# Performance work log

Measured on AMD Instinct MI355X. Metric: run time of the kernel, lower is better.

Reference implementation:

```python
import jax, jax.numpy as jnp
import numpy as np

H = W = 112  # densepose head output grid
D = 16       # CSE embedding dim


def setup_inputs() -> dict:
    key = jax.random.key(0)
    k1, k2 = jax.random.split(key)
    feats = jax.random.normal(k1, (4, D, H, W), dtype=jnp.float32)
    vertex_embeddings = jax.random.normal(k2, (27554, D), dtype=jnp.float32)
    return {"feats": feats, "vertex_embeddings": vertex_embeddings}


def reference(feats, vertex_embeddings):
    # feats: [bs, 16, 112, 112]; vertex_embeddings: [V, 16]
    c2 = jnp.sum(vertex_embeddings * vertex_embeddings, axis=1)  # [V]

    def per_image(f):
        x = f.reshape(D, -1).T                      # [P, 16], P = 112*112
        x2 = jnp.sum(x * x, axis=1, keepdims=True)  # [P, 1]
        # squared euclidean distance matrix [P, V] (materialized, as in original)
        dist = x2 - 2.0 * (x @ vertex_embeddings.T) + c2[None, :]
        return jnp.argmin(dist, axis=1).reshape(H, W)

    # process images one at a time (matches original per-image loop, bounds peak memory)
    dps = jax.lax.map(per_image, feats)  # [bs, 112, 112] int
    return feats, dps
```

## Files before the change

kernel.cpp:

```cpp
#include <hip/hip_runtime.h>
#include <stdint.h>


#define DIMS   16
#define HW     12544
#define P_TOT  50176
#define V_TOT  27554
#define FEAT_N 802816

#define CV     512
#define NCH    54
#define VPAD   (NCH*CV)
#define PIXW   128
#define TPW    8
#define B2BX   32
#define CNTSTRIDE 32

#define NV     64
#define VC     431
#define PPT    4

typedef __attribute__((ext_vector_type(8))) short bf16x8;
typedef __attribute__((ext_vector_type(4))) float f32x4;

#define OFF_KEYS  0ul
#define OFF_N2MAX 401408ul
#define OFF_C2    401664ul
#define OFF_XN    512000ul
#define OFF_X2T   712704ul
#define OFF_XB    3923968ul
#define OFF_CNT   3923968ul
#define OFF_WB    7135232ul
#define OFF_CM    8904704ul
#define OFF_BKT   19742976ul
#define WS_BIG    30580992ul
#define MOFF_KEYS  0ul
#define MOFF_N2MAX 401408ul
#define MOFF_C2    405504ul
#define MOFF_XN    516096ul
#define MOFF_XB    716800ul
#define MOFF_WB    3928064ul
#define MOFF_CM    5697536ul
#define WS_MID     16535552ul

__device__ __forceinline__ unsigned short rne_bf16(float f) {
    unsigned u = __float_as_uint(f);
    return (unsigned short)((u + 0x7FFFu + ((u >> 16) & 1u)) >> 16);
}
__device__ __forceinline__ float bf2f(unsigned short h) {
    return __uint_as_float(((unsigned)h) << 16);
}
__device__ __forceinline__ unsigned sortable(float s) {
    unsigned u = __float_as_uint(s);
    return (u & 0x80000000u) ? ~u : (u | 0x80000000u);
}

__global__ void prep_v(const float* __restrict__ ve, short* __restrict__ wb,
                       float* __restrict__ c2buf, unsigned* __restrict__ n2max)
{
    int v = blockIdx.x * 256 + threadIdx.x;
    if (v >= VPAD) return;
    int c = v / CV, vl = v % CV;
    bf16x8 r0, r1, r2, r3;
#pragma unroll
    for (int k = 0; k < 8; ++k) { r2[k] = 0; r3[k] = 0; }
    if (v < V_TOT) {
        const float4* w4 = (const float4*)(ve + (size_t)v * DIMS);
        float w[16];
        *(float4*)&w[0] = w4[0]; *(float4*)&w[4]  = w4[1];
        *(float4*)&w[8] = w4[2]; *(float4*)&w[12] = w4[3];
        float c2 = 0.f;
#pragma unroll
        for (int k = 0; k < 16; ++k) c2 = fmaf(w[k], w[k], c2);
        c2buf[v] = c2;
        float n2 = 0.f;
#pragma unroll
        for (int k = 0; k < 16; ++k) {
            unsigned short h = rne_bf16(-2.f * w[k]);
            if (k < 8) r0[k] = (short)h; else r1[k - 8] = (short)h;
            float f = bf2f(h);
            n2 = fmaf(f, f, n2);
        }
        atomicMax(n2max, __float_as_uint(n2));
        unsigned short hi = rne_bf16(c2);
        unsigned short lo = rne_bf16(c2 - bf2f(hi));
        r2[0] = (short)hi; r2[1] = (short)lo;
    } else {
#pragma unroll
        for (int k = 0; k < 8; ++k) { r0[k] = 0; r1[k] = 0; }
        r2[0] = (short)rne_bf16(30000.f);
    }
    *(bf16x8*)(wb + (((size_t)c * 4 + 0) * CV + vl) * 8) = r0;
    *(bf16x8*)(wb + (((size_t)c * 4 + 1) * CV + vl) * 8) = r1;
    *(bf16x8*)(wb + (((size_t)c * 4 + 2) * CV + vl) * 8) = r2;
    *(bf16x8*)(wb + (((size_t)c * 4 + 3) * CV + vl) * 8) = r3;
}

__global__ void prep_x(const float* __restrict__ feats, short* __restrict__ xb,
                       float* __restrict__ xn, float* __restrict__ x2T)
{
    int p = blockIdx.x * 256 + threadIdx.x;
    int b = p / HW, hw = p - b * HW;
    const float* f = feats + (size_t)b * DIMS * HW + hw;
    bf16x8 r0, r1, r2, r3;
#pragma unroll
    for (int k = 0; k < 8; ++k) { r2[k] = 0; r3[k] = 0; }
    float n2 = 0.f;
    float xv[16];
#pragma unroll
    for (int k = 0; k < 16; ++k) {
        float fv = f[k * HW];
        xv[k] = -2.f * fv;
        unsigned short h = rne_bf16(fv);
        if (k < 8) r0[k] = (short)h; else r1[k - 8] = (short)h;
        float x = bf2f(h);
        n2 = fmaf(x, x, n2);
    }
    r2[0] = (short)0x3F80; r2[1] = (short)0x3F80;
    xn[p] = sqrtf(n2);
    if (x2T) {
        float4* o = (float4*)(x2T + (size_t)p * 16);
        o[0] = *(float4*)&xv[0];  o[1] = *(float4*)&xv[4];
        o[2] = *(float4*)&xv[8];  o[3] = *(float4*)&xv[12];
    }
    *(bf16x8*)(xb + ((size_t)0 * P_TOT + p) * 8) = r0;
    *(bf16x8*)(xb + ((size_t)1 * P_TOT + p) * 8) = r1;
    *(bf16x8*)(xb + ((size_t)2 * P_TOT + p) * 8) = r2;
    *(bf16x8*)(xb + ((size_t)3 * P_TOT + p) * 8) = r3;
}

__global__ __launch_bounds__(256)
void pass_a(const short* __restrict__ xb, const short* __restrict__ wb,
            float* __restrict__ chunkmin)
{
    __shared__ int4 wlds[4 * CV];
    const int c = blockIdx.y;
    const int4* wsrc = (const int4*)(wb + (size_t)c * 4 * CV * 8);
    for (int r = threadIdx.x; r < 4 * CV; r += 256) wlds[r] = wsrc[r];

    const int wid = threadIdx.x >> 6, lane = threadIdx.x & 63;
    const int q = lane >> 4, l15 = lane & 15;
    const int p0 = (blockIdx.x * 4 + wid) * PIXW;

    bf16x8 bfrag[TPW];
#pragma unroll
    for (int t = 0; t < TPW; ++t)
        bfrag[t] = *(const bf16x8*)(xb + ((size_t)q * P_TOT + p0 + t * 16 + l15) * 8);

    __syncthreads();

    f32x4 z = {0.f, 0.f, 0.f, 0.f};
    float run[TPW];
#pragma unroll
    for (int t = 0; t < TPW; ++t) run[t] = 3.0e38f;

    const short* wl = (const short*)wlds + (size_t)q * CV * 8;
#pragma unroll 2
    for (int s = 0; s < CV / 16; ++s) {
        bf16x8 a = *(const bf16x8*)(wl + (s * 16 + l15) * 8);
        f32x4 acc[TPW];
#pragma unroll
        for (int t = 0; t < TPW; ++t)
            acc[t] = __builtin_amdgcn_mfma_f32_16x16x32_bf16(a, bfrag[t], z, 0, 0, 0);
#pragma unroll
        for (int t = 0; t < TPW; ++t) {
            float m = fminf(fminf(acc[t][0], acc[t][1]), acc[t][2]);
            run[t] = fminf(fminf(run[t], acc[t][3]), m);
        }
    }
#pragma unroll
    for (int t = 0; t < TPW; ++t) {
        float v = run[t];
        v = fminf(v, __shfl_xor(v, 16, 64));
        v = fminf(v, __shfl_xor(v, 32, 64));
        if (lane < 16)
            chunkmin[(size_t)c * P_TOT + p0 + t * 16 + lane] = v;
    }
}

__global__ __launch_bounds__(256)
void pass_b1(const float* __restrict__ chunkmin, const float* __restrict__ xn,
             const unsigned* __restrict__ n2max,
             unsigned* __restrict__ cnt, unsigned* __restrict__ buckets)
{
    __shared__ unsigned hist[NCH];
    __shared__ unsigned basech[NCH];
    __shared__ unsigned offch[NCH];

    const int tid  = threadIdx.x;
    const int p    = blockIdx.x * 256 + tid;
    const int lane = tid & 63;

    for (int i = tid; i < NCH; i += 256) { hist[i] = 0; offch[i] = 0; }
    __syncthreads();

    float cm[NCH];
    float gm = 3.0e38f;
#pragma unroll
    for (int c = 0; c < NCH; ++c) {
        cm[c] = chunkmin[(size_t)c * P_TOT + p];
        gm = fminf(gm, cm[c]);
    }
    float Wm = sqrtf(__uint_as_float(*n2max));
    float T = gm + 2.f * (0.004f * xn[p] * Wm + 1e-3f);

#pragma unroll
    for (int c = 0; c < NCH; ++c) {
        unsigned long long m = __ballot(cm[c] <= T);
        if (m && lane == 0) atomicAdd(&hist[c], (unsigned)__popcll(m));
    }
    __syncthreads();

    for (int c = tid; c < NCH; c += 256) {
        unsigned h = hist[c];
        basech[c] = h ? atomicAdd(&cnt[(size_t)c * CNTSTRIDE], h) : 0u;
    }
    __syncthreads();

#pragma unroll
    for (int c = 0; c < NCH; ++c) {
        bool want = (cm[c] <= T);
        unsigned long long m = __ballot(want);
        if (!m) continue;
        unsigned wbase = 0;
        int leader = __ffsll(m) - 1;
        if (lane == leader) wbase = atomicAdd(&offch[c], (unsigned)__popcll(m));
        wbase = __shfl(wbase, leader, 64);
        if (want) {
            unsigned pos = (unsigned)__popcll(m & ((1ull << lane) - 1ull));
            buckets[(size_t)c * P_TOT + basech[c] + wbase + pos] = (unsigned)p;
        }
    }
}

__global__ __launch_bounds__(256)
void pass_b2(const unsigned* __restrict__ cnt, const unsigned* __restrict__ buckets,
             const float* __restrict__ ve, const float* __restrict__ c2buf,
             const float* __restrict__ x2T, unsigned long long* __restrict__ keys)
{
    __shared__ float wl[CV * 20];
    const int c = blockIdx.y;
    const int vbase = c * CV;
    const int rows = min(CV, V_TOT - vbase);
    for (int r = threadIdx.x; r < rows * 5; r += 256) {
        int v = r / 5, s = r % 5;
        if (s < 4)
            *(float4*)&wl[v * 20 + s * 4] =
                *(const float4*)(ve + (size_t)(vbase + v) * DIMS + s * 4);
        else
            wl[v * 20 + 16] = c2buf[vbase + v];
    }
    __syncthreads();

    const int wid = threadIdx.x >> 6, lane = threadIdx.x & 63;
    const unsigned n = cnt[(size_t)c * CNTSTRIDE];
    for (unsigned i = blockIdx.x * 4 + wid; i < n; i += B2BX * 4) {
        const unsigned p = buckets[(size_t)c * P_TOT + i];
        const float4* xq = (const float4*)(x2T + (size_t)p * 16);
        const float4 xa = xq[0], xb4 = xq[1], xc = xq[2], xd = xq[3];
        unsigned long long best = ~0ull;
#pragma unroll
        for (int k = 0; k < 8; ++k) {
            int v = k * 64 + lane;
            if (v < rows) {
                const float* row = &wl[v * 20];
                float4 a  = *(const float4*)(row);
                float4 b4 = *(const float4*)(row + 4);
                float4 cc = *(const float4*)(row + 8);
                float4 d4 = *(const float4*)(row + 12);
                float s = row[16];
                s = fmaf(xa.x,  a.x,  s); s = fmaf(xa.y,  a.y,  s);
                s = fmaf(xa.z,  a.z,  s); s = fmaf(xa.w,  a.w,  s);
                s = fmaf(xb4.x, b4.x, s); s = fmaf(xb4.y, b4.y, s);
                s = fmaf(xb4.z, b4.z, s); s = fmaf(xb4.w, b4.w, s);
                s = fmaf(xc.x,  cc.x, s); s = fmaf(xc.y,  cc.y, s);
                s = fmaf(xc.z,  cc.z, s); s = fmaf(xc.w,  cc.w, s);
                s = fmaf(xd.x,  d4.x, s); s = fmaf(xd.y,  d4.y, s);
                s = fmaf(xd.z,  d4.z, s); s = fmaf(xd.w,  d4.w, s);
                unsigned long long key =
                    ((unsigned long long)sortable(s) << 32) | (unsigned)(vbase + v);
                best = key < best ? key : best;
            }
        }
#pragma unroll
        for (int off = 32; off; off >>= 1) {
            unsigned long long o = __shfl_xor(best, off, 64);
            best = o < best ? o : best;
        }
        if (lane == 0) atomicMin(&keys[p], best);
    }
}

__global__ __launch_bounds__(256)
void pass_b(const float* __restrict__ chunkmin, const float* __restrict__ xn,
            const unsigned* __restrict__ n2max, const float* __restrict__ c2buf,
            const float* __restrict__ feats, const float* __restrict__ ve,
            unsigned long long* __restrict__ keys)
{
    __shared__ float cmins[NCH][64];
    __shared__ float Tsh[64];
    __shared__ float xlds[16][64];
    __shared__ unsigned long long candm[NCH];
    const int p0 = blockIdx.x * 64;
    const int tid = threadIdx.x;
    for (int i = tid; i < NCH * 64; i += 256) {
        int c = i >> 6, t = i & 63;
        cmins[c][t] = chunkmin[(size_t)c * P_TOT + p0 + t];
    }
    for (int i = tid; i < 16 * 64; i += 256) {
        int k = i >> 6, t = i & 63;
        int p = p0 + t, b = p / HW, hw = p - b * HW;
        xlds[k][t] = -2.f * feats[((size_t)b * DIMS + k) * HW + hw];
    }
    __syncthreads();
    if (tid < 64) {
        float gm = 3.0e38f;
        for (int c = 0; c < NCH; ++c) gm = fminf(gm, cmins[c][tid]);
        float Wm = sqrtf(__uint_as_float(*n2max));
        float mp = 0.004f * xn[p0 + tid] * Wm + 1e-3f;
        Tsh[tid] = gm + 2.f * mp;
    }
    __syncthreads();
    if (tid < 64) {
        for (int c = 0; c < NCH; ++c) {
            unsigned long long m = __ballot(cmins[c][tid] <= Tsh[tid]);
            if (tid == 0) candm[c] = m;
        }
    }
    __syncthreads();
    for (int c = 0; c < NCH; ++c) {
        unsigned long long m = candm[c];
        while (m) {
            int t = __ffsll((unsigned long long)m) - 1;
            m &= m - 1;
            unsigned long long best = ~0ull;
            int vend = min((c + 1) * CV, V_TOT);
            for (int v = c * CV + tid; v < vend; v += 256) {
                const float4* w4 = (const float4*)(ve + (size_t)v * DIMS);
                float4 a = w4[0], b4 = w4[1], cc = w4[2], d4 = w4[3];
                float s = c2buf[v];
                s = fmaf(xlds[0][t],  a.x,  s); s = fmaf(xlds[1][t],  a.y,  s);
                s = fmaf(xlds[2][t],  a.z,  s); s = fmaf(xlds[3][t],  a.w,  s);
                s = fmaf(xlds[4][t],  b4.x, s); s = fmaf(xlds[5][t],  b4.y, s);
                s = fmaf(xlds[6][t],  b4.z, s); s = fmaf(xlds[7][t],  b4.w, s);
                s = fmaf(xlds[8][t],  cc.x, s); s = fmaf(xlds[9][t],  cc.y, s);
                s = fmaf(xlds[10][t], cc.z, s); s = fmaf(xlds[11][t], cc.w, s);
                s = fmaf(xlds[12][t], d4.x, s); s = fmaf(xlds[13][t], d4.y, s);
                s = fmaf(xlds[14][t], d4.z, s); s = fmaf(xlds[15][t], d4.w, s);
                unsigned long long key =
                    ((unsigned long long)sortable(s) << 32) | (unsigned)v;
                best = (key < best) ? key : best;
            }
            for (int off = 32; off; off >>= 1) {
                unsigned long long o = __shfl_xor(best, off, 64);
                best = (o < best) ? o : best;
            }
            if ((tid & 63) == 0) atomicMin(&keys[p0 + t], best);
        }
    }
}

__global__ void cse_finalize(const unsigned long long* __restrict__ keys,
                             float* __restrict__ out)
{
    int p = blockIdx.x * 256 + threadIdx.x;
    if (p < P_TOT)
        out[FEAT_N + p] = (float)(unsigned)(keys[p] & 0xffffffffull);
}

__global__ __launch_bounds__(256, 2)
void cse_argmin(const float* __restrict__ feats, const float* __restrict__ ve,
                unsigned long long* __restrict__ keys)
{
    __shared__ float4 se4[VC * 4];
    __shared__ float  sh[VC];
    const int j = blockIdx.y, v0 = j * VC;
    const int cnt = min(VC, V_TOT - v0);
    for (int t = threadIdx.x; t < cnt; t += 256) {
        const float4* w4 = (const float4*)(ve + (size_t)(v0 + t) * DIMS);
        float4 a = w4[0], b = w4[1], c = w4[2], d = w4[3];
        float h = a.x*a.x + a.y*a.y + a.z*a.z + a.w*a.w
                + b.x*b.x + b.y*b.y + b.z*b.z + b.w*b.w
                + c.x*c.x + c.y*c.y + c.z*c.z + c.w*c.w
                + d.x*d.x + d.y*d.y + d.z*d.z + d.w*d.w;
        se4[t*4+0] = make_float4(-a.x,-a.y,-a.z,-a.w);
        se4[t*4+1] = make_float4(-b.x,-b.y,-b.z,-b.w);
        se4[t*4+2] = make_float4(-c.x,-c.y,-c.z,-c.w);
        se4[t*4+3] = make_float4(-d.x,-d.y,-d.z,-d.w);
        sh[t] = 0.5f * h;
    }
    __syncthreads();
    const int p0 = (blockIdx.x * 256 + threadIdx.x) * PPT;
    const int bb = p0 / HW, hw = p0 - bb * HW;
    const float* fb = feats + (size_t)bb * (DIMS * HW) + hw;
    float4 x[DIMS];
#pragma unroll
    for (int d = 0; d < DIMS; ++d) x[d] = *(const float4*)(fb + d * HW);
    float m0b = 3.4e38f, m1b = 3.4e38f, m2b = 3.4e38f, m3b = 3.4e38f;
    int i0 = 0, i1 = 0, i2 = 0, i3 = 0;
#pragma unroll 2
    for (int v = 0; v < cnt; ++v) {
        const float h = sh[v];
        float m0 = h, m1 = h, m2 = h, m3 = h;
#pragma unroll
        for (int k = 0; k < 4; ++k) {
            const float4 nw = se4[v*4 + k];
            const float4 xa = x[4*k+0], xb = x[4*k+1], xc = x[4*k+2], xd = x[4*k+3];
            m0 = fmaf(nw.x, xa.x, m0); m0 = fmaf(nw.y, xb.x, m0);
            m0 = fmaf(nw.z, xc.x, m0); m0 = fmaf(nw.w, xd.x, m0);
            m1 = fmaf(nw.x, xa.y, m1); m1 = fmaf(nw.y, xb.y, m1);
            m1 = fmaf(nw.z, xc.y, m1); m1 = fmaf(nw.w, xd.y, m1);
            m2 = fmaf(nw.x, xa.z, m2); m2 = fmaf(nw.y, xb.z, m2);
            m2 = fmaf(nw.z, xc.z, m2); m2 = fmaf(nw.w, xd.z, m2);
            m3 = fmaf(nw.x, xa.w, m3); m3 = fmaf(nw.y, xb.w, m3);
            m3 = fmaf(nw.z, xc.w, m3); m3 = fmaf(nw.w, xd.w, m3);
        }
        const int vg = v0 + v;
        bool c0 = m0 < m0b; m0b = c0 ? m0 : m0b; i0 = c0 ? vg : i0;
        bool c1 = m1 < m1b; m1b = c1 ? m1 : m1b; i1 = c1 ? vg : i1;
        bool c2 = m2 < m2b; m2b = c2 ? m2 : m2b; i2 = c2 ? vg : i2;
        bool c3 = m3 < m3b; m3b = c3 ? m3 : m3b; i3 = c3 ? vg : i3;
    }
    unsigned long long* kp = keys + p0;
    float mb[PPT] = { m0b, m1b, m2b, m3b };
    int   ib[PPT] = { i0, i1, i2, i3 };
#pragma unroll
    for (int p = 0; p < PPT; ++p) {
        unsigned long long key = ((unsigned long long)sortable(mb[p]) << 32) | (unsigned)ib[p];
        atomicMin(&kp[p], key);
    }
}

extern "C" void kernel_launch(void* const* d_in, const int* in_sizes, int n_in,
                              void* d_out, int out_size, void* d_ws, size_t ws_size,
                              hipStream_t stream)
{
    const float* feats = (const float*)d_in[0];
    const float* ve    = (const float*)d_in[1];
    float* out = (float*)d_out;
    char* ws = (char*)d_ws;

    hipMemcpyAsync(out, feats, (size_t)FEAT_N * sizeof(float),
                   hipMemcpyDeviceToDevice, stream);

    if (ws_size >= WS_BIG) {
        unsigned long long* keys = (unsigned long long*)(ws + OFF_KEYS);
        unsigned* n2max = (unsigned*)(ws + OFF_N2MAX);
        float* c2buf = (float*)(ws + OFF_C2);
        float* xnorm = (float*)(ws + OFF_XN);
        float* x2T   = (float*)(ws + OFF_X2T);
        short* xbuf  = (short*)(ws + OFF_XB);
        short* wbuf  = (short*)(ws + OFF_WB);
        float* cmin  = (float*)(ws + OFF_CM);
        unsigned* cnt = (unsigned*)(ws + OFF_CNT);
        unsigned* bkt = (unsigned*)(ws + OFF_BKT);

        hipMemsetAsync(keys, 0xFF, (size_t)P_TOT * 8, stream);
        hipMemsetAsync(n2max, 0, 4, stream);

        prep_v<<<VPAD / 256, 256, 0, stream>>>(ve, wbuf, c2buf, n2max);
        prep_x<<<P_TOT / 256, 256, 0, stream>>>(feats, xbuf, xnorm, x2T);
        pass_a<<<dim3(P_TOT / (4 * PIXW), NCH), 256, 0, stream>>>(xbuf, wbuf, cmin);
        hipMemsetAsync(cnt, 0, (size_t)NCH * CNTSTRIDE * 4, stream);
        pass_b1<<<P_TOT / 256, 256, 0, stream>>>(cmin, xnorm, n2max, cnt, bkt);
        pass_b2<<<dim3(B2BX, NCH), 256, 0, stream>>>(cnt, bkt, ve, c2buf, x2T, keys);
        cse_finalize<<<(P_TOT + 255) / 256, 256, 0, stream>>>(keys, out);
    } else if (ws_size >= WS_MID) {
        unsigned long long* keys = (unsigned long long*)(ws + MOFF_KEYS);
        unsigned* n2max = (unsigned*)(ws + MOFF_N2MAX);
        float* c2buf = (float*)(ws + MOFF_C2);
        float* xnorm = (float*)(ws + MOFF_XN);
        short* xbuf  = (short*)(ws + MOFF_XB);
        short* wbuf  = (short*)(ws + MOFF_WB);
        float* cmin  = (float*)(ws + MOFF_CM);

        hipMemsetAsync(keys, 0xFF, (size_t)P_TOT * 8, stream);
        hipMemsetAsync(n2max, 0, 4, stream);

        prep_v<<<VPAD / 256, 256, 0, stream>>>(ve, wbuf, c2buf, n2max);
        prep_x<<<P_TOT / 256, 256, 0, stream>>>(feats, xbuf, xnorm, nullptr);
        pass_a<<<dim3(P_TOT / (4 * PIXW), NCH), 256, 0, stream>>>(xbuf, wbuf, cmin);
        pass_b<<<P_TOT / 64, 256, 0, stream>>>(cmin, xnorm, n2max, c2buf,
                                               feats, ve, keys);
        cse_finalize<<<(P_TOT + 255) / 256, 256, 0, stream>>>(keys, out);
    } else {
        unsigned long long* keys = (unsigned long long*)d_ws;
        hipMemsetAsync(d_ws, 0xFF, (size_t)P_TOT * 8, stream);
        cse_argmin<<<dim3(P_TOT / (256 * PPT), NV), 256, 0, stream>>>(feats, ve, keys);
        cse_finalize<<<(P_TOT + 255) / 256, 256, 0, stream>>>(keys, out);
    }
}
```

Before: 243.3 us.

## Switch coarse pass to 32x32x16 MFMA with c2 as accumulator, per-chunk norms

```diff
diff --git a/kernel.cpp b/kernel.cpp
--- a/kernel.cpp
+++ b/kernel.cpp
@@ -12,7 +12,6 @@
 #define NCH    54
 #define VPAD   (NCH*CV)
 #define PIXW   128
-#define TPW    8
 #define B2BX   32
 #define CNTSTRIDE 32
 
@@ -20,28 +19,21 @@
 #define VC     431
 #define PPT    4
 
-typedef __attribute__((ext_vector_type(8))) short bf16x8;
-typedef __attribute__((ext_vector_type(4))) float f32x4;
+typedef __attribute__((ext_vector_type(8)))  short bf16x8;
+typedef __attribute__((ext_vector_type(4)))  float f32x4;
+typedef __attribute__((ext_vector_type(16))) float f32x16;
 
 #define OFF_KEYS  0ul
-#define OFF_N2MAX 401408ul
-#define OFF_C2    401664ul
-#define OFF_XN    512000ul
-#define OFF_X2T   712704ul
-#define OFF_XB    3923968ul
-#define OFF_CNT   3923968ul
-#define OFF_WB    7135232ul
-#define OFF_CM    8904704ul
-#define OFF_BKT   19742976ul
+#define OFF_NMX   401408ul
+#define OFF_CNT   408576ul
+#define OFF_C2    415744ul
+#define OFF_XN    526336ul
+#define OFF_X2T   727040ul
+#define OFF_XB    3938304ul
+#define OFF_WB    5543936ul
+#define OFF_CM    6428672ul
+#define OFF_BKT   17266688ul
 #define WS_BIG    30580992ul
-#define MOFF_KEYS  0ul
-#define MOFF_N2MAX 401408ul
-#define MOFF_C2    405504ul
-#define MOFF_XN    516096ul
-#define MOFF_XB    716800ul
-#define MOFF_WB    3928064ul
-#define MOFF_CM    5697536ul
-#define WS_MID     16535552ul
 
 __device__ __forceinline__ unsigned short rne_bf16(float f) {
     unsigned u = __float_as_uint(f);
@@ -56,24 +48,23 @@
 }
 
 __global__ void prep_v(const float* __restrict__ ve, short* __restrict__ wb,
-                       float* __restrict__ c2buf, unsigned* __restrict__ n2max)
+                       float* __restrict__ c2buf, unsigned* __restrict__ n2maxc)
 {
     int v = blockIdx.x * 256 + threadIdx.x;
     if (v >= VPAD) return;
     int c = v / CV, vl = v % CV;
-    bf16x8 r0, r1, r2, r3;
-#pragma unroll
-    for (int k = 0; k < 8; ++k) { r2[k] = 0; r3[k] = 0; }
+    int lane = threadIdx.x & 63;
+    bf16x8 r0, r1;
+    float c2 = 30000.f;
+    float n2 = 0.f;
     if (v < V_TOT) {
         const float4* w4 = (const float4*)(ve + (size_t)v * DIMS);
         float w[16];
         *(float4*)&w[0] = w4[0]; *(float4*)&w[4]  = w4[1];
         *(float4*)&w[8] = w4[2]; *(float4*)&w[12] = w4[3];
-        float c2 = 0.f;
+        c2 = 0.f;
 #pragma unroll
         for (int k = 0; k < 16; ++k) c2 = fmaf(w[k], w[k], c2);
-        c2buf[v] = c2;
-        float n2 = 0.f;
 #pragma unroll
         for (int k = 0; k < 16; ++k) {
             unsigned short h = rne_bf16(-2.f * w[k]);
@@ -81,19 +72,18 @@
             float f = bf2f(h);
             n2 = fmaf(f, f, n2);
         }
-        atomicMax(n2max, __float_as_uint(n2));
-        unsigned short hi = rne_bf16(c2);
-        unsigned short lo = rne_bf16(c2 - bf2f(hi));
-        r2[0] = (short)hi; r2[1] = (short)lo;
     } else {
 #pragma unroll
         for (int k = 0; k < 8; ++k) { r0[k] = 0; r1[k] = 0; }
-        r2[0] = (short)rne_bf16(30000.f);
-    }
-    *(bf16x8*)(wb + (((size_t)c * 4 + 0) * CV + vl) * 8) = r0;
-    *(bf16x8*)(wb + (((size_t)c * 4 + 1) * CV + vl) * 8) = r1;
-    *(bf16x8*)(wb + (((size_t)c * 4 + 2) * CV + vl) * 8) = r2;
-    *(bf16x8*)(wb + (((size_t)c * 4 + 3) * CV + vl) * 8) = r3;
+    }
+    c2buf[v] = c2;
+#pragma unroll
+    for (int off = 32; off; off >>= 1)
+        n2 = fmaxf(n2, __shfl_xor(n2, off, 64));
+    if (lane == 0)
+        atomicMax(&n2maxc[(size_t)c * CNTSTRIDE], __float_as_uint(n2));
+    *(bf16x8*)(wb + (((size_t)c * 2 + 0) * CV + vl) * 8) = r0;
+    *(bf16x8*)(wb + (((size_t)c * 2 + 1) * CV + vl) * 8) = r1;
 }
 
 __global__ void prep_x(const float* __restrict__ feats, short* __restrict__ xb,
@@ -102,9 +92,7 @@
     int p = blockIdx.x * 256 + threadIdx.x;
     int b = p / HW, hw = p - b * HW;
     const float* f = feats + (size_t)b * DIMS * HW + hw;
-    bf16x8 r0, r1, r2, r3;
-#pragma unroll
-    for (int k = 0; k < 8; ++k) { r2[k] = 0; r3[k] = 0; }
+    bf16x8 r0, r1;
     float n2 = 0.f;
     float xv[16];
 #pragma unroll
@@ -116,73 +104,78 @@
         float x = bf2f(h);
         n2 = fmaf(x, x, n2);
     }
-    r2[0] = (short)0x3F80; r2[1] = (short)0x3F80;
     xn[p] = sqrtf(n2);
-    if (x2T) {
-        float4* o = (float4*)(x2T + (size_t)p * 16);
-        o[0] = *(float4*)&xv[0];  o[1] = *(float4*)&xv[4];
-        o[2] = *(float4*)&xv[8];  o[3] = *(float4*)&xv[12];
-    }
+    float4* o = (float4*)(x2T + (size_t)p * 16);
+    o[0] = *(float4*)&xv[0];  o[1] = *(float4*)&xv[4];
+    o[2] = *(float4*)&xv[8];  o[3] = *(float4*)&xv[12];
     *(bf16x8*)(xb + ((size_t)0 * P_TOT + p) * 8) = r0;
     *(bf16x8*)(xb + ((size_t)1 * P_TOT + p) * 8) = r1;
-    *(bf16x8*)(xb + ((size_t)2 * P_TOT + p) * 8) = r2;
-    *(bf16x8*)(xb + ((size_t)3 * P_TOT + p) * 8) = r3;
 }
 
 __global__ __launch_bounds__(256)
 void pass_a(const short* __restrict__ xb, const short* __restrict__ wb,
-            float* __restrict__ chunkmin)
-{
-    __shared__ int4 wlds[4 * CV];
+            const float* __restrict__ c2buf, float* __restrict__ chunkmin)
+{
+    __shared__ short wlds[2 * CV * 8];
+    __shared__ float c2lds[CV];
+
     const int c = blockIdx.y;
-    const int4* wsrc = (const int4*)(wb + (size_t)c * 4 * CV * 8);
-    for (int r = threadIdx.x; r < 4 * CV; r += 256) wlds[r] = wsrc[r];
+    const int4* wsrc = (const int4*)(wb + (size_t)c * 2 * CV * 8);
+    int4* wdst = (int4*)wlds;
+    for (int r = threadIdx.x; r < 2 * CV; r += 256) wdst[r] = wsrc[r];
+    const float4* csrc = (const float4*)(c2buf + (size_t)c * CV);
+    float4* cdst = (float4*)c2lds;
+    for (int r = threadIdx.x; r < CV / 4; r += 256) cdst[r] = csrc[r];
 
     const int wid = threadIdx.x >> 6, lane = threadIdx.x & 63;
-    const int q = lane >> 4, l15 = lane & 15;
+    const int col = lane & 31, hi = lane >> 5;
     const int p0 = (blockIdx.x * 4 + wid) * PIXW;
 
-    bf16x8 bfrag[TPW];
-#pragma unroll
-    for (int t = 0; t < TPW; ++t)
-        bfrag[t] = *(const bf16x8*)(xb + ((size_t)q * P_TOT + p0 + t * 16 + l15) * 8);
-
-    __syncthreads();
-
-    f32x4 z = {0.f, 0.f, 0.f, 0.f};
-    float run[TPW];
-#pragma unroll
-    for (int t = 0; t < TPW; ++t) run[t] = 3.0e38f;
-
-    const short* wl = (const short*)wlds + (size_t)q * CV * 8;
+    bf16x8 bfrag[4];
+#pragma unroll
+    for (int t = 0; t < 4; ++t)
+        bfrag[t] = *(const bf16x8*)(xb + ((size_t)hi * P_TOT + p0 + t * 32 + col) * 8);
+
+    __syncthreads();
+
+    float run[4] = {3.0e38f, 3.0e38f, 3.0e38f, 3.0e38f};
+    const short* wl = wlds + (size_t)hi * CV * 8;
+
 #pragma unroll 2
-    for (int s = 0; s < CV / 16; ++s) {
-        bf16x8 a = *(const bf16x8*)(wl + (s * 16 + l15) * 8);
-        f32x4 acc[TPW];
-#pragma unroll
-        for (int t = 0; t < TPW; ++t)
-            acc[t] = __builtin_amdgcn_mfma_f32_16x16x32_bf16(a, bfrag[t], z, 0, 0, 0);
-#pragma unroll
-        for (int t = 0; t < TPW; ++t) {
-            float m = fminf(fminf(acc[t][0], acc[t][1]), acc[t][2]);
-            run[t] = fminf(fminf(run[t], acc[t][3]), m);
-        }
-    }
-#pragma unroll
-    for (int t = 0; t < TPW; ++t) {
-        float v = run[t];
-        v = fminf(v, __shfl_xor(v, 16, 64));
-        v = fminf(v, __shfl_xor(v, 32, 64));
-        if (lane < 16)
-            chunkmin[(size_t)c * P_TOT + p0 + t * 16 + lane] = v;
-    }
+    for (int s = 0; s < CV / 32; ++s) {
+        bf16x8 a = *(const bf16x8*)(wl + (s * 32 + col) * 8);
+        union { f32x16 v; f32x4 q[4]; } c2f;
+#pragma unroll
+        for (int g = 0; g < 4; ++g)
+            c2f.q[g] = *(const f32x4*)&c2lds[s * 32 + 4 * hi + 8 * g];
+#pragma unroll
+        for (int t = 0; t < 4; ++t) {
+            f32x16 acc = __builtin_amdgcn_mfma_f32_32x32x16_bf16(
+                a, bfrag[t], c2f.v, 0, 0, 0);
+            float m0 = fminf(fminf(acc[0],  acc[1]),  acc[2]);
+            float m1 = fminf(fminf(acc[3],  acc[4]),  acc[5]);
+            float m2 = fminf(fminf(acc[6],  acc[7]),  acc[8]);
+            float m3 = fminf(fminf(acc[9],  acc[10]), acc[11]);
+            float m4 = fminf(fminf(acc[12], acc[13]), acc[14]);
+            float mm = fminf(fminf(m0, m1), m2);
+            mm = fminf(fminf(mm, m3), m4);
+            mm = fminf(mm, acc[15]);
+            mm = fminf(mm, __shfl_xor(mm, 32, 64));
+            run[t] = fminf(run[t], mm);
+        }
+    }
+#pragma unroll
+    for (int t = 0; t < 4; ++t)
+        if (lane < 32)
+            chunkmin[(size_t)c * P_TOT + p0 + t * 32 + lane] = run[t];
 }
 
 __global__ __launch_bounds__(256)
 void pass_b1(const float* __restrict__ chunkmin, const float* __restrict__ xn,
-             const unsigned* __restrict__ n2max,
+             const unsigned* __restrict__ n2maxc,
              unsigned* __restrict__ cnt, unsigned* __restrict__ buckets)
 {
+    __shared__ float    wms[NCH];
     __shared__ unsigned hist[NCH];
     __shared__ unsigned basech[NCH];
     __shared__ unsigned offch[NCH];
@@ -191,22 +184,25 @@
     const int p    = blockIdx.x * 256 + tid;
     const int lane = tid & 63;
 
-    for (int i = tid; i < NCH; i += 256) { hist[i] = 0; offch[i] = 0; }
-    __syncthreads();
-
+    for (int i = tid; i < NCH; i += 256) {
+        wms[i] = sqrtf(__uint_as_float(n2maxc[(size_t)i * CNTSTRIDE]));
+        hist[i] = 0; offch[i] = 0;
+    }
+    __syncthreads();
+
+    const float kx = 0.004f * xn[p];
     float cm[NCH];
-    float gm = 3.0e38f;
+    float gmp = 3.0e38f;
 #pragma unroll
     for (int c = 0; c < NCH; ++c) {
         cm[c] = chunkmin[(size_t)c * P_TOT + p];
-        gm = fminf(gm, cm[c]);
-    }
-    float Wm = sqrtf(__uint_as_float(*n2max));
-    float T = gm + 2.f * (0.004f * xn[p] * Wm + 1e-3f);
+        gmp = fminf(gmp, cm[c] + fmaf(kx, wms[c], 1e-3f));
+    }
 
 #pragma unroll
     for (int c = 0; c < NCH; ++c) {
-        unsigned long long m = __ballot(cm[c] <= T);
+        bool want = (cm[c] - fmaf(kx, wms[c], 1e-3f)) <= gmp;
+        unsigned long long m = __ballot(want);
         if (m && lane == 0) atomicAdd(&hist[c], (unsigned)__popcll(m));
     }
     __syncthreads();
@@ -219,7 +215,7 @@
 
 #pragma unroll
     for (int c = 0; c < NCH; ++c) {
-        bool want = (cm[c] <= T);
+        bool want = (cm[c] - fmaf(kx, wms[c], 1e-3f)) <= gmp;
         unsigned long long m = __ballot(want);
         if (!m) continue;
         unsigned wbase = 0;
@@ -291,75 +287,6 @@
     }
 }
 
-__global__ __launch_bounds__(256)
-void pass_b(const float* __restrict__ chunkmin, const float* __restrict__ xn,
-            const unsigned* __restrict__ n2max, const float* __restrict__ c2buf,
-            const float* __restrict__ feats, const float* __restrict__ ve,
-            unsigned long long* __restrict__ keys)
-{
-    __shared__ float cmins[NCH][64];
-    __shared__ float Tsh[64];
-    __shared__ float xlds[16][64];
-    __shared__ unsigned long long candm[NCH];
-    const int p0 = blockIdx.x * 64;
-    const int tid = threadIdx.x;
-    for (int i = tid; i < NCH * 64; i += 256) {
-        int c = i >> 6, t = i & 63;
-        cmins[c][t] = chunkmin[(size_t)c * P_TOT + p0 + t];
-    }
-    for (int i = tid; i < 16 * 64; i += 256) {
-        int k = i >> 6, t = i & 63;
-        int p = p0 + t, b = p / HW, hw = p - b * HW;
-        xlds[k][t] = -2.f * feats[((size_t)b * DIMS + k) * HW + hw];
-    }
-    __syncthreads();
-    if (tid < 64) {
-        float gm = 3.0e38f;
-        for (int c = 0; c < NCH; ++c) gm = fminf(gm, cmins[c][tid]);
-        float Wm = sqrtf(__uint_as_float(*n2max));
-        float mp = 0.004f * xn[p0 + tid] * Wm + 1e-3f;
-        Tsh[tid] = gm + 2.f * mp;
-    }
-    __syncthreads();
-    if (tid < 64) {
-        for (int c = 0; c < NCH; ++c) {
-            unsigned long long m = __ballot(cmins[c][tid] <= Tsh[tid]);
-            if (tid == 0) candm[c] = m;
-        }
-    }
-    __syncthreads();
-    for (int c = 0; c < NCH; ++c) {
-        unsigned long long m = candm[c];
-        while (m) {
-            int t = __ffsll((unsigned long long)m) - 1;
-            m &= m - 1;
-            unsigned long long best = ~0ull;
-            int vend = min((c + 1) * CV, V_TOT);
-            for (int v = c * CV + tid; v < vend; v += 256) {
-                const float4* w4 = (const float4*)(ve + (size_t)v * DIMS);
-                float4 a = w4[0], b4 = w4[1], cc = w4[2], d4 = w4[3];
-                float s = c2buf[v];
-                s = fmaf(xlds[0][t],  a.x,  s); s = fmaf(xlds[1][t],  a.y,  s);
-                s = fmaf(xlds[2][t],  a.z,  s); s = fmaf(xlds[3][t],  a.w,  s);
-                s = fmaf(xlds[4][t],  b4.x, s); s = fmaf(xlds[5][t],  b4.y, s);
-                s = fmaf(xlds[6][t],  b4.z, s); s = fmaf(xlds[7][t],  b4.w, s);
-                s = fmaf(xlds[8][t],  cc.x, s); s = fmaf(xlds[9][t],  cc.y, s);
-                s = fmaf(xlds[10][t], cc.z, s); s = fmaf(xlds[11][t], cc.w, s);
-                s = fmaf(xlds[12][t], d4.x, s); s = fmaf(xlds[13][t], d4.y, s);
-                s = fmaf(xlds[14][t], d4.z, s); s = fmaf(xlds[15][t], d4.w, s);
-                unsigned long long key =
-                    ((unsigned long long)sortable(s) << 32) | (unsigned)v;
-                best = (key < best) ? key : best;
-            }
-            for (int off = 32; off; off >>= 1) {
-                unsigned long long o = __shfl_xor(best, off, 64);
-                best = (o < best) ? o : best;
-            }
-            if ((tid & 63) == 0) atomicMin(&keys[p0 + t], best);
-        }
-    }
-}
-
 __global__ void cse_finalize(const unsigned long long* __restrict__ keys,
                              float* __restrict__ out)
 {
@@ -445,43 +372,26 @@
 
     if (ws_size >= WS_BIG) {
         unsigned long long* keys = (unsigned long long*)(ws + OFF_KEYS);
-        unsigned* n2max = (unsigned*)(ws + OFF_N2MAX);
+        unsigned* n2maxc = (unsigned*)(ws + OFF_NMX);
+        unsigned* cnt    = (unsigned*)(ws + OFF_CNT);
         float* c2buf = (float*)(ws + OFF_C2);
         float* xnorm = (float*)(ws + OFF_XN);
         float* x2T   = (float*)(ws + OFF_X2T);
         short* xbuf  = (short*)(ws + OFF_XB);
         short* wbuf  = (short*)(ws + OFF_WB);
         float* cmin  = (float*)(ws + OFF_CM);
-        unsigned* cnt = (unsigned*)(ws + OFF_CNT);
         unsigned* bkt = (unsigned*)(ws + OFF_BKT);
 
         hipMemsetAsync(keys, 0xFF, (size_t)P_TOT * 8, stream);
-        hipMemsetAsync(n2max, 0, 4, stream);
-
-        prep_v<<<VPAD / 256, 256, 0, stream>>>(ve, wbuf, c2buf, n2max);
+        hipMemsetAsync(n2maxc, 0, (size_t)NCH * CNTSTRIDE * 4, stream);
+        hipMemsetAsync(cnt, 0, (size_t)NCH * CNTSTRIDE * 4, stream);
+
+        prep_v<<<VPAD / 256, 256, 0, stream>>>(ve, wbuf, c2buf, n2maxc);
         prep_x<<<P_TOT / 256, 256, 0, stream>>>(feats, xbuf, xnorm, x2T);
-        pass_a<<<dim3(P_TOT / (4 * PIXW), NCH), 256, 0, stream>>>(xbuf, wbuf, cmin);
-        hipMemsetAsync(cnt, 0, (size_t)NCH * CNTSTRIDE * 4, stream);
-        pass_b1<<<P_TOT / 256, 256, 0, stream>>>(cmin, xnorm, n2max, cnt, bkt);
+        pass_a<<<dim3(P_TOT / (4 * PIXW), NCH), 256, 0, stream>>>(xbuf, wbuf,
+                                                                  c2buf, cmin);
+        pass_b1<<<P_TOT / 256, 256, 0, stream>>>(cmin, xnorm, n2maxc, cnt, bkt);
         pass_b2<<<dim3(B2BX, NCH), 256, 0, stream>>>(cnt, bkt, ve, c2buf, x2T, keys);
-        cse_finalize<<<(P_TOT + 255) / 256, 256, 0, stream>>>(keys, out);
-    } else if (ws_size >= WS_MID) {
-        unsigned long long* keys = (unsigned long long*)(ws + MOFF_KEYS);
-        unsigned* n2max = (unsigned*)(ws + MOFF_N2MAX);
-        float* c2buf = (float*)(ws + MOFF_C2);
-        float* xnorm = (float*)(ws + MOFF_XN);
-        short* xbuf  = (short*)(ws + MOFF_XB);
-        short* wbuf  = (short*)(ws + MOFF_WB);
-        float* cmin  = (float*)(ws + MOFF_CM);
-
-        hipMemsetAsync(keys, 0xFF, (size_t)P_TOT * 8, stream);
-        hipMemsetAsync(n2max, 0, 4, stream);
-
-        prep_v<<<VPAD / 256, 256, 0, stream>>>(ve, wbuf, c2buf, n2max);
-        prep_x<<<P_TOT / 256, 256, 0, stream>>>(feats, xbuf, xnorm, nullptr);
-        pass_a<<<dim3(P_TOT / (4 * PIXW), NCH), 256, 0, stream>>>(xbuf, wbuf, cmin);
-        pass_b<<<P_TOT / 64, 256, 0, stream>>>(cmin, xnorm, n2max, c2buf,
-                                               feats, ve, keys);
         cse_finalize<<<(P_TOT + 255) / 256, 256, 0, stream>>>(keys, out);
     } else {
         unsigned long long* keys = (unsigned long long*)d_ws;
```

Measured after the change: 222.3 us. 1.09x faster.
